# Kernel tuning notes

Measured on AMD Instinct MI355X. Metric: run time of the kernel, lower is better.

The kernel has to match this reference:

```python
import jax, jax.numpy as jnp
import numpy as np

N_NODES = 51 * 51 * 51  # 132651, from h,w,d = (51,51,51)
AVG_DEG = 64
N_EDGES = N_NODES * AVG_DEG  # 8489664 (even, required by view([2, E//2]))


def setup_inputs() -> dict:
    key = jax.random.key(0)
    k1, k2, k3, k4 = jax.random.split(key, 4)
    x = jax.random.normal(k1, (N_NODES, 1), dtype=jnp.float32)
    W = jax.random.normal(k2, (1, 2), dtype=jnp.float32)  # GCNConv weight (in=1, out=2)
    b = jax.random.normal(k3, (2,), dtype=jnp.float32)    # GCNConv bias
    edge_index = jax.random.randint(k4, (2, N_EDGES), 0, N_NODES, dtype=jnp.int64)
    return {"x": x, "W": W, "b": b, "edge_index": edge_index}


def reference(x, W, b, edge_index):
    N = x.shape[0]
    row, col = edge_index[0], edge_index[1]  # source -> target (PyG flow)

    loop = jnp.arange(N, dtype=edge_index.dtype)
    row_sl = jnp.concatenate([row, loop])
    col_sl = jnp.concatenate([col, loop])
    deg = jax.ops.segment_sum(jnp.ones_like(col_sl, dtype=x.dtype), col_sl, num_segments=N)
    dinv = jnp.where(deg > 0, jax.lax.rsqrt(jnp.maximum(deg, 1e-12)), 0.0)
    norm = dinv[row_sl] * dinv[col_sl]  # [E + N]

    xw = x @ W  # [N, 2]
    msg = norm[:, None] * xw[row_sl]  # gather + scale
    h = jax.ops.segment_sum(msg, col_sl, num_segments=N) + b  # scatter-add aggregate
    h = jax.nn.relu(h)  # [N, 2]

    # Per-edge: sum over channels of endpoint features, fold halves, sigmoid
    y = jnp.sum(h[row] + h[col], axis=-1)           # [E]
    y = jnp.mean(y.reshape(2, -1), axis=0)[:, None]  # [E//2, 1]
    return jax.nn.sigmoid(y)
```

## Files before the change

### kernel.cpp

```cpp
#include <hip/hip_runtime.h>
#include <hip/hip_bf16.h>
#include <math.h>

constexpr int N_NODES = 51 * 51 * 51;
constexpr int N_EDGES = N_NODES * 64;
constexpr int E_HALF  = N_EDGES / 2;
constexpr int NP      = (N_NODES + 255) & ~255;

constexpr int WORDS_D8 = 36864;
constexpr int PART_S2 = 73728;
constexpr int NP_S2   = 2;
constexpr int PART_O   = 73728;
constexpr int SH_LEN   = PART_O * 2;
constexpr int OUT_BLOCKS = 256;

__device__ __forceinline__ float h2f(ushort u) {
    return (float)__builtin_bit_cast(_Float16, u);
}
__device__ __forceinline__ ushort f2h(float f) {
    return __builtin_bit_cast(unsigned short, (_Float16)f);
}


__global__ __launch_bounds__(1024) void k_deg8(const int4* __restrict__ col4,
                                               unsigned* __restrict__ partial,
                                               int Bp) {
    __shared__ unsigned cnt[WORDS_D8];
    for (int j = threadIdx.x; j < WORDS_D8; j += 1024) cnt[j] = 0u;
    __syncthreads();
    const int n4 = N_EDGES / 4;
    const int stride = Bp * 1024;
    int i = blockIdx.x * 1024 + threadIdx.x;
    bool valid = i < n4;
    int4 c;
    if (valid) c = col4[i];
    while (valid) {
        const int inext = i + stride;
        const bool vnext = inext < n4;
        int4 cn;
        if (vnext) cn = col4[inext];
        atomicAdd(&cnt[(unsigned)c.x >> 2], 1u << (((unsigned)c.x & 3u) << 3));
        atomicAdd(&cnt[(unsigned)c.y >> 2], 1u << (((unsigned)c.y & 3u) << 3));
        atomicAdd(&cnt[(unsigned)c.z >> 2], 1u << (((unsigned)c.z & 3u) << 3));
        atomicAdd(&cnt[(unsigned)c.w >> 2], 1u << (((unsigned)c.w & 3u) << 3));
        c = cn; i = inext; valid = vnext;
    }
    __syncthreads();
    uint4* dst = (uint4*)(partial + (size_t)blockIdx.x * WORDS_D8);
    const uint4* src = (const uint4*)cnt;
    for (int j = threadIdx.x; j < WORDS_D8 / 4; j += 1024) dst[j] = src[j];
}

__global__ __launch_bounds__(256) void k_reduceA(const unsigned* __restrict__ partial,
                                                 const float* __restrict__ x,
                                                 int Bp,
                                                 float* __restrict__ dinv,
                                                 float* __restrict__ uf,
                                                 ushort* __restrict__ uh) {
    int v = blockIdx.x * 256 + threadIdx.x;
    if (v >= N_NODES) return;
    const unsigned* src = partial + ((unsigned)v >> 2);
    const int sh = ((unsigned)v & 3u) << 3;
    unsigned deg = 1;
#pragma unroll 8
    for (int b = 0; b < Bp; ++b) deg += (src[(size_t)b * WORDS_D8] >> sh) & 0xFFu;
    float d = rsqrtf((float)deg);
    dinv[v] = d;
    float uu = d * x[v];
    uf[v] = uu;
    uh[v] = f2h(uu);
}

__global__ __launch_bounds__(1024) void k_scat2(const int4* __restrict__ row4,
                                                const int4* __restrict__ col4,
                                                const ushort* __restrict__ uh,
                                                ushort* __restrict__ partialH,
                                                int Bp) {
    __shared__ unsigned acc[PART_S2 / 2];
    const int p = blockIdx.x / Bp;
    const int b = blockIdx.x % Bp;
    const int base = p * PART_S2;
    for (int j = threadIdx.x; j < PART_S2 / 2; j += 1024) acc[j] = 0u;
    __syncthreads();
    const unsigned accBase = (unsigned)(uintptr_t)(&acc[0]);
    const int n4 = N_EDGES / 4;
    const int stride = Bp * 1024;
    const int step2 = 2 * stride;

#define GATH1(JJ, GG, CC, RR)                                                  \
    unsigned JJ = (unsigned)((CC) - base);                                     \
    ushort GG = 0;                                                             \
    if (JJ < (unsigned)PART_S2) GG = uh[RR];
#define DSADD(JJ, GG)                                                          \
    if (JJ < (unsigned)PART_S2) {                                              \
        unsigned pk = (unsigned)(GG) << ((JJ & 1u) << 4);                      \
        unsigned off = accBase + ((JJ >> 1) << 2);                             \
        asm volatile("ds_pk_add_f16 %0, %1" :: "v"(off), "v"(pk));             \
    }

#pragma unroll 2
    for (int i = b * 1024 + threadIdx.x; i < n4; i += step2) {
        const int iB = i + stride;
        const bool vB = iB < n4;
        int4 cA = col4[i];
        int4 rA = row4[i];
        int4 cB, rB;
        if (vB) { cB = col4[iB]; rB = row4[iB]; }
        else    { cB = make_int4(-1, -1, -1, -1); rB = make_int4(0, 0, 0, 0); }
        GATH1(jax, gax, cA.x, rA.x) GATH1(jay, gay, cA.y, rA.y)
        GATH1(jaz, gaz, cA.z, rA.z) GATH1(jaw, gaw, cA.w, rA.w)
        GATH1(jbx, gbx, cB.x, rB.x) GATH1(jby, gby, cB.y, rB.y)
        GATH1(jbz, gbz, cB.z, rB.z) GATH1(jbw, gbw, cB.w, rB.w)
        DSADD(jax, gax) DSADD(jay, gay) DSADD(jaz, gaz) DSADD(jaw, gaw)
        DSADD(jbx, gbx) DSADD(jby, gby) DSADD(jbz, gbz) DSADD(jbw, gbw)
    }
#undef GATH1
#undef DSADD

    __syncthreads();
    uint4* dst = (uint4*)(partialH + (size_t)blockIdx.x * PART_S2);
    const uint4* src = (const uint4*)acc;
    for (int j = threadIdx.x; j < PART_S2 / 8; j += 1024) dst[j] = src[j];
}

__global__ __launch_bounds__(256) void k_reduceB(const ushort* __restrict__ partialH,
                                                 const float* __restrict__ dinv,
                                                 const float* __restrict__ uf,
                                                 const float* __restrict__ W,
                                                 const float* __restrict__ bb,
                                                 int Bp,
                                                 ushort* __restrict__ sh) {
    int v = blockIdx.x * 256 + threadIdx.x;
    if (v >= N_NODES) return;
    const int p = (v >= PART_S2) ? 1 : 0;
    const int j = v - p * PART_S2;
    const ushort* src = partialH + (size_t)(p * Bp) * PART_S2 + j;
    float g = 0.f;
#pragma unroll 8
    for (int b = 0; b < Bp; ++b) g += h2f(src[(size_t)b * PART_S2]);
    float t = dinv[v] * (g + uf[v]);
    float h0 = fmaxf(fmaf(t, W[0], bb[0]), 0.f);
    float h1 = fmaxf(fmaf(t, W[1], bb[1]), 0.f);
    sh[v] = f2h(h0 + h1);
}


__global__ __launch_bounds__(256) void k_init_deg(int* __restrict__ deg) {
    int i = blockIdx.x * 256 + threadIdx.x;
    if (i < N_NODES) deg[i] = 1;
}

__global__ __launch_bounds__(256) void k_deg(const int4* __restrict__ col4,
                                             int* __restrict__ deg) {
    int i = blockIdx.x * 256 + threadIdx.x;
    const int stride = gridDim.x * 256;
    const int n4 = N_EDGES / 4;
    for (; i < n4; i += stride) {
        int4 c = col4[i];
        atomicAdd(&deg[c.x], 1); atomicAdd(&deg[c.y], 1);
        atomicAdd(&deg[c.z], 1); atomicAdd(&deg[c.w], 1);
    }
}

__global__ __launch_bounds__(256) void k_dinv(const int* __restrict__ deg,
                                              const float* __restrict__ x,
                                              float* __restrict__ dinv,
                                              float* __restrict__ t) {
    int i = blockIdx.x * 256 + threadIdx.x;
    if (i >= N_NODES) return;
    float d = rsqrtf((float)deg[i]);
    dinv[i] = d;
    t[i] = d * d * x[i];
}

__global__ __launch_bounds__(256) void k_scatter(const int4* __restrict__ row4,
                                                 const int4* __restrict__ col4,
                                                 const float* __restrict__ x,
                                                 const float* __restrict__ dinv,
                                                 float* __restrict__ t) {
    int i = blockIdx.x * 256 + threadIdx.x;
    const int stride = gridDim.x * 256;
    const int n4 = N_EDGES / 4;
    for (; i < n4; i += stride) {
        int4 r = row4[i];
        int4 c = col4[i];
        atomicAdd(&t[c.x], dinv[r.x] * dinv[c.x] * x[r.x]);
        atomicAdd(&t[c.y], dinv[r.y] * dinv[c.y] * x[r.y]);
        atomicAdd(&t[c.z], dinv[r.z] * dinv[c.z] * x[r.z]);
        atomicAdd(&t[c.w], dinv[r.w] * dinv[c.w] * x[r.w]);
    }
}

__global__ __launch_bounds__(256) void k_node(const float* __restrict__ t,
                                              const float* __restrict__ W,
                                              const float* __restrict__ b,
                                              ushort* __restrict__ sh) {
    int i = blockIdx.x * 256 + threadIdx.x;
    if (i >= N_NODES) return;
    float tv = t[i];
    float h0 = fmaxf(fmaf(tv, W[0], b[0]), 0.f);
    float h1 = fmaxf(fmaf(tv, W[1], b[1]), 0.f);
    sh[i] = f2h(h0 + h1);
}


__global__ __launch_bounds__(1024) void k_out_pass(const int4* __restrict__ rowA4,
                                                   const int4* __restrict__ colA4,
                                                   const int4* __restrict__ rowB4,
                                                   const int4* __restrict__ colB4,
                                                   const ushort* __restrict__ sh,
                                                   float4* __restrict__ out,
                                                   int base, int final_pass) {
    __shared__ ushort sl[PART_O];
    {
        const uint4* src = (const uint4*)(sh + base);
        uint4* dst = (uint4*)sl;
        for (int j = threadIdx.x; j < PART_O / 8; j += 1024) dst[j] = src[j];
    }
    __syncthreads();
    const int n4 = E_HALF / 4;
    const int stride = gridDim.x * 1024;
#pragma unroll 2
    for (int i = blockIdx.x * 1024 + threadIdx.x; i < n4; i += stride) {
        int4 ra = rowA4[i], ca = colA4[i], rb = rowB4[i], cb = colB4[i];
        float c0 = 0.f, c1 = 0.f, c2 = 0.f, c3 = 0.f;
        unsigned j;
        j = (unsigned)(ra.x - base); if (j < (unsigned)PART_O) c0 += h2f(sl[j]);
        j = (unsigned)(ca.x - base); if (j < (unsigned)PART_O) c0 += h2f(sl[j]);
        j = (unsigned)(rb.x - base); if (j < (unsigned)PART_O) c0 += h2f(sl[j]);
        j = (unsigned)(cb.x - base); if (j < (unsigned)PART_O) c0 += h2f(sl[j]);
        j = (unsigned)(ra.y - base); if (j < (unsigned)PART_O) c1 += h2f(sl[j]);
        j = (unsigned)(ca.y - base); if (j < (unsigned)PART_O) c1 += h2f(sl[j]);
        j = (unsigned)(rb.y - base); if (j < (unsigned)PART_O) c1 += h2f(sl[j]);
        j = (unsigned)(cb.y - base); if (j < (unsigned)PART_O) c1 += h2f(sl[j]);
        j = (unsigned)(ra.z - base); if (j < (unsigned)PART_O) c2 += h2f(sl[j]);
        j = (unsigned)(ca.z - base); if (j < (unsigned)PART_O) c2 += h2f(sl[j]);
        j = (unsigned)(rb.z - base); if (j < (unsigned)PART_O) c2 += h2f(sl[j]);
        j = (unsigned)(cb.z - base); if (j < (unsigned)PART_O) c2 += h2f(sl[j]);
        j = (unsigned)(ra.w - base); if (j < (unsigned)PART_O) c3 += h2f(sl[j]);
        j = (unsigned)(ca.w - base); if (j < (unsigned)PART_O) c3 += h2f(sl[j]);
        j = (unsigned)(rb.w - base); if (j < (unsigned)PART_O) c3 += h2f(sl[j]);
        j = (unsigned)(cb.w - base); if (j < (unsigned)PART_O) c3 += h2f(sl[j]);
        float4 o;
        if (final_pass) {
            float4 prev = out[i];
            o.x = 1.f / (1.f + __expf(-0.5f * (prev.x + c0)));
            o.y = 1.f / (1.f + __expf(-0.5f * (prev.y + c1)));
            o.z = 1.f / (1.f + __expf(-0.5f * (prev.z + c2)));
            o.w = 1.f / (1.f + __expf(-0.5f * (prev.w + c3)));
        } else {
            o.x = c0; o.y = c1; o.z = c2; o.w = c3;
        }
        out[i] = o;
    }
}


extern "C" void kernel_launch(void* const* d_in, const int* in_sizes, int n_in,
                              void* d_out, int out_size, void* d_ws, size_t ws_size,
                              hipStream_t stream) {
    const float* x = (const float*)d_in[0];
    const float* W = (const float*)d_in[1];
    const float* b = (const float*)d_in[2];
    const int*   ei = (const int*)d_in[3];
    const int* row = ei;
    const int* col = ei + N_EDGES;
    float* out = (float*)d_out;

    char* ws = (char*)d_ws;
    float*  dinv = (float*)(ws);
    float*  uf   = (float*)(ws + (size_t)NP * 4);
    ushort* uh   = (ushort*)(ws + (size_t)NP * 8);
    ushort* sh   = (ushort*)(ws + (size_t)NP * 10);
    char* partialBase = ws + (size_t)NP * 10 + (size_t)SH_LEN * 2;
    size_t head = (size_t)NP * 10 + (size_t)SH_LEN * 2;
    size_t avail = (ws_size > head) ? ws_size - head : 0;

    int Bp_d = (int)(avail / 147456);
    if (Bp_d > 256) Bp_d = 256;
    int Bp_s = (int)(avail / (2 * 147456));
    if (Bp_s > 128) Bp_s = 128;

    const int nodeBlocks = (N_NODES + 255) / 256;
    const int edgeBlocks = 2048;

    if (Bp_s >= 2 && Bp_d >= 2) {
        unsigned* partU = (unsigned*)partialBase;
        ushort*   partH = (ushort*)partialBase;
        k_deg8<<<Bp_d, 1024, 0, stream>>>((const int4*)col, partU, Bp_d);
        k_reduceA<<<nodeBlocks, 256, 0, stream>>>(partU, x, Bp_d, dinv, uf, uh);
        k_scat2<<<NP_S2 * Bp_s, 1024, 0, stream>>>((const int4*)row, (const int4*)col,
                                                   uh, partH, Bp_s);
        k_reduceB<<<nodeBlocks, 256, 0, stream>>>(partH, dinv, uf, W, b, Bp_s, sh);
    } else {
        int* deg = (int*)partialBase;
        k_init_deg<<<nodeBlocks, 256, 0, stream>>>(deg);
        k_deg<<<edgeBlocks, 256, 0, stream>>>((const int4*)col, deg);
        k_dinv<<<nodeBlocks, 256, 0, stream>>>(deg, x, dinv, uf);
        k_scatter<<<edgeBlocks, 256, 0, stream>>>((const int4*)row, (const int4*)col,
                                                  x, dinv, uf);
        k_node<<<nodeBlocks, 256, 0, stream>>>(uf, W, b, sh);
    }

    k_out_pass<<<OUT_BLOCKS, 1024, 0, stream>>>(
        (const int4*)row, (const int4*)col,
        (const int4*)(row + E_HALF), (const int4*)(col + E_HALF),
        sh, (float4*)out, 0, 0);
    k_out_pass<<<OUT_BLOCKS, 1024, 0, stream>>>(
        (const int4*)row, (const int4*)col,
        (const int4*)(row + E_HALF), (const int4*)(col + E_HALF),
        sh, (float4*)out, PART_O, 1);
}
```

Measured before the change: 136.4 us.

## Split degree histogram into two node passes and scatter into four smaller partitions

The degree-counting kernel now runs two node-range passes, each with a 73728-node 8-bit-packed LDS histogram instead of one 147456-node table, so each block uses half the shared memory (18432 words). The scatter kernel partitions nodes into four 36864-node ranges instead of two 73728-node ranges, halving its LDS footprint. Smaller LDS use should let more blocks run per CU and raise occupancy for the atomic-heavy loops. The cost is that every edge index is read more times (twice for degrees, four times for scatter), and the partial-buffer block counts change with workspace size.

```diff
diff --git a/kernel.cpp b/kernel.cpp
--- a/kernel.cpp
+++ b/kernel.cpp
@@ -7,9 +7,11 @@
 constexpr int E_HALF  = N_EDGES / 2;
 constexpr int NP      = (N_NODES + 255) & ~255;
 
-constexpr int WORDS_D8 = 36864;
-constexpr int PART_S2 = 73728;
-constexpr int NP_S2   = 2;
+constexpr int PART_D8  = 73728;
+constexpr int WORDS_D8 = PART_D8 / 4;
+constexpr int NPASS_D  = 2;
+constexpr int PART_S  = 36864;
+constexpr int NP_S    = 4;
 constexpr int PART_O   = 73728;
 constexpr int SH_LEN   = PART_O * 2;
 constexpr int OUT_BLOCKS = 256;
@@ -26,11 +28,14 @@
                                                unsigned* __restrict__ partial,
                                                int Bp) {
     __shared__ unsigned cnt[WORDS_D8];
+    const int p = blockIdx.x / Bp;
+    const int b = blockIdx.x % Bp;
+    const int base = p * PART_D8;
     for (int j = threadIdx.x; j < WORDS_D8; j += 1024) cnt[j] = 0u;
     __syncthreads();
     const int n4 = N_EDGES / 4;
     const int stride = Bp * 1024;
-    int i = blockIdx.x * 1024 + threadIdx.x;
+    int i = b * 1024 + threadIdx.x;
     bool valid = i < n4;
     int4 c;
     if (valid) c = col4[i];
@@ -39,10 +44,15 @@
         const bool vnext = inext < n4;
         int4 cn;
         if (vnext) cn = col4[inext];
-        atomicAdd(&cnt[(unsigned)c.x >> 2], 1u << (((unsigned)c.x & 3u) << 3));
-        atomicAdd(&cnt[(unsigned)c.y >> 2], 1u << (((unsigned)c.y & 3u) << 3));
-        atomicAdd(&cnt[(unsigned)c.z >> 2], 1u << (((unsigned)c.z & 3u) << 3));
-        atomicAdd(&cnt[(unsigned)c.w >> 2], 1u << (((unsigned)c.w & 3u) << 3));
+        unsigned j;
+        j = (unsigned)(c.x - base);
+        if (j < (unsigned)PART_D8) atomicAdd(&cnt[j >> 2], 1u << ((j & 3u) << 3));
+        j = (unsigned)(c.y - base);
+        if (j < (unsigned)PART_D8) atomicAdd(&cnt[j >> 2], 1u << ((j & 3u) << 3));
+        j = (unsigned)(c.z - base);
+        if (j < (unsigned)PART_D8) atomicAdd(&cnt[j >> 2], 1u << ((j & 3u) << 3));
+        j = (unsigned)(c.w - base);
+        if (j < (unsigned)PART_D8) atomicAdd(&cnt[j >> 2], 1u << ((j & 3u) << 3));
         c = cn; i = inext; valid = vnext;
     }
     __syncthreads();
@@ -59,8 +69,10 @@
                                                  ushort* __restrict__ uh) {
     int v = blockIdx.x * 256 + threadIdx.x;
     if (v >= N_NODES) return;
-    const unsigned* src = partial + ((unsigned)v >> 2);
-    const int sh = ((unsigned)v & 3u) << 3;
+    const int p = (v >= PART_D8) ? 1 : 0;
+    const int j = v - p * PART_D8;
+    const int sh = (j & 3) << 3;
+    const unsigned* src = partial + (size_t)(p * Bp) * WORDS_D8 + (j >> 2);
     unsigned deg = 1;
 #pragma unroll 8
     for (int b = 0; b < Bp; ++b) deg += (src[(size_t)b * WORDS_D8] >> sh) & 0xFFu;
@@ -76,11 +88,11 @@
                                                 const ushort* __restrict__ uh,
                                                 ushort* __restrict__ partialH,
                                                 int Bp) {
-    __shared__ unsigned acc[PART_S2 / 2];
+    __shared__ unsigned acc[PART_S / 2];
     const int p = blockIdx.x / Bp;
     const int b = blockIdx.x % Bp;
-    const int base = p * PART_S2;
-    for (int j = threadIdx.x; j < PART_S2 / 2; j += 1024) acc[j] = 0u;
+    const int base = p * PART_S;
+    for (int j = threadIdx.x; j < PART_S / 2; j += 1024) acc[j] = 0u;
     __syncthreads();
     const unsigned accBase = (unsigned)(uintptr_t)(&acc[0]);
     const int n4 = N_EDGES / 4;
@@ -90,9 +102,9 @@
 #define GATH1(JJ, GG, CC, RR)                                                  \
     unsigned JJ = (unsigned)((CC) - base);                                     \
     ushort GG = 0;                                                             \
-    if (JJ < (unsigned)PART_S2) GG = uh[RR];
+    if (JJ < (unsigned)PART_S) GG = uh[RR];
 #define DSADD(JJ, GG)                                                          \
-    if (JJ < (unsigned)PART_S2) {                                              \
+    if (JJ < (unsigned)PART_S) {                                               \
         unsigned pk = (unsigned)(GG) << ((JJ & 1u) << 4);                      \
         unsigned off = accBase + ((JJ >> 1) << 2);                             \
         asm volatile("ds_pk_add_f16 %0, %1" :: "v"(off), "v"(pk));             \
@@ -118,9 +130,9 @@
 #undef DSADD
 
     __syncthreads();
-    uint4* dst = (uint4*)(partialH + (size_t)blockIdx.x * PART_S2);
+    uint4* dst = (uint4*)(partialH + (size_t)blockIdx.x * PART_S);
     const uint4* src = (const uint4*)acc;
-    for (int j = threadIdx.x; j < PART_S2 / 8; j += 1024) dst[j] = src[j];
+    for (int j = threadIdx.x; j < PART_S / 8; j += 1024) dst[j] = src[j];
 }
 
 __global__ __launch_bounds__(256) void k_reduceB(const ushort* __restrict__ partialH,
@@ -132,12 +144,12 @@
                                                  ushort* __restrict__ sh) {
     int v = blockIdx.x * 256 + threadIdx.x;
     if (v >= N_NODES) return;
-    const int p = (v >= PART_S2) ? 1 : 0;
-    const int j = v - p * PART_S2;
-    const ushort* src = partialH + (size_t)(p * Bp) * PART_S2 + j;
+    const int p = (unsigned)v / (unsigned)PART_S;
+    const int j = v - p * PART_S;
+    const ushort* src = partialH + (size_t)(p * Bp) * PART_S + j;
     float g = 0.f;
 #pragma unroll 8
-    for (int b = 0; b < Bp; ++b) g += h2f(src[(size_t)b * PART_S2]);
+    for (int b = 0; b < Bp; ++b) g += h2f(src[(size_t)b * PART_S]);
     float t = dinv[v] * (g + uf[v]);
     float h0 = fmaxf(fmaf(t, W[0], bb[0]), 0.f);
     float h1 = fmaxf(fmaf(t, W[1], bb[1]), 0.f);
@@ -276,9 +288,9 @@
     size_t head = (size_t)NP * 10 + (size_t)SH_LEN * 2;
     size_t avail = (ws_size > head) ? ws_size - head : 0;
 
-    int Bp_d = (int)(avail / 147456);
+    int Bp_d = (int)(avail / ((size_t)NPASS_D * 73728));
     if (Bp_d > 256) Bp_d = 256;
-    int Bp_s = (int)(avail / (2 * 147456));
+    int Bp_s = (int)(avail / ((size_t)NP_S * 73728));
     if (Bp_s > 128) Bp_s = 128;
 
     const int nodeBlocks = (N_NODES + 255) / 256;
@@ -287,10 +299,10 @@
     if (Bp_s >= 2 && Bp_d >= 2) {
         unsigned* partU = (unsigned*)partialBase;
         ushort*   partH = (ushort*)partialBase;
-        k_deg8<<<Bp_d, 1024, 0, stream>>>((const int4*)col, partU, Bp_d);
+        k_deg8<<<NPASS_D * Bp_d, 1024, 0, stream>>>((const int4*)col, partU, Bp_d);
         k_reduceA<<<nodeBlocks, 256, 0, stream>>>(partU, x, Bp_d, dinv, uf, uh);
-        k_scat2<<<NP_S2 * Bp_s, 1024, 0, stream>>>((const int4*)row, (const int4*)col,
-                                                   uh, partH, Bp_s);
+        k_scat2<<<NP_S * Bp_s, 1024, 0, stream>>>((const int4*)row, (const int4*)col,
+                                                  uh, partH, Bp_s);
         k_reduceB<<<nodeBlocks, 256, 0, stream>>>(partH, dinv, uf, W, b, Bp_s, sh);
     } else {
         int* deg = (int*)partialBase;
```

Measured after the change: 136.6 us. About the same (+0.2%).
